# Kernel optimization log

Hardware: AMD Instinct MI355X
Metric: run time of the kernel (lower is better)

## Reference

```python
import jax, jax.numpy as jnp
import numpy as np

# static config (mirrors params)
T, B, NA, NF = 48, 256, 23, 4
D = NA * NF          # y_dim = 92
XD = 2               # x_dim
H = 128              # rnn_dim
HD = 128             # h_dim
NL = 2               # n_layers
FS = 0.1
BURN = 12
IN_ENC = XD + D + H  # GRU input size = 222
A0, A1 = 12, 11      # agents 0..11 -> net0, 12..22 -> net1


def setup_inputs() -> dict:
    key = jax.random.key(0)
    ks = jax.random.split(key, 16)
    s = 0.05
    rn = lambda k, shape: jax.random.normal(k, shape, jnp.float32) * s
    return {
        "states": jax.random.normal(ks[0], (T + 1, 1, B, D), jnp.float32),
        # per-network (leading dim 2) GRU layer-0 and layer-1 weights (torch GRU layout: [r|z|n])
        "W_ih0": rn(ks[1], (2, 3 * H, IN_ENC)),
        "W_hh0": rn(ks[2], (2, 3 * H, H)),
        "b_ih0": rn(ks[3], (2, 3 * H)),
        "b_hh0": rn(ks[4], (2, 3 * H)),
        "W_ih1": rn(ks[5], (2, 3 * H, H)),
        "W_hh1": rn(ks[6], (2, 3 * H, H)),
        "b_ih1": rn(ks[7], (2, 3 * H)),
        "b_hh1": rn(ks[8], (2, 3 * H)),
        # decoder MLP (dropout is identity in eval) + mean head
        "W1": rn(ks[9], (2, HD, H)),
        "b1": rn(ks[10], (2, HD)),
        "W2": rn(ks[11], (2, HD, HD)),
        "b2": rn(ks[12], (2, HD)),
        "Wm": rn(ks[13], (2, XD, HD)),
        "bm": rn(ks[14], (2, XD)),
        "rollout": 0,
        "train": 0,
    }


def _gru_cell(x, h, Wih, Whh, bih, bhh):
    gi = x @ Wih.T + bih
    gh = h @ Whh.T + bhh
    r = jax.nn.sigmoid(gi[:, :H] + gh[:, :H])
    z = jax.nn.sigmoid(gi[:, H:2 * H] + gh[:, H:2 * H])
    n = jnp.tanh(gi[:, 2 * H:] + r * gh[:, 2 * H:])
    return (1.0 - z) * n + z * h


def _batch_error(a, b):
    # sum over batch of the euclidean norm over features
    return jnp.sum(jnp.sqrt(jnp.sum((a - b) ** 2, axis=1)))


def _group_step(h, y_t, y3, y3n, lo, hi, g, P):
    # h: [NL, A*B, H]; agents lo..hi-1 of network g, folded into the batch dim
    A = hi - lo
    vel = y3[:, lo:hi, 2:4].transpose(1, 0, 2).reshape(A * B, 2)
    pos = y3[:, lo:hi, 0:2].transpose(1, 0, 2).reshape(A * B, 2)
    vel_true = y3n[:, lo:hi, 2:4].transpose(1, 0, 2).reshape(A * B, 2)
    pos_true = y3n[:, lo:hi, 0:2].transpose(1, 0, 2).reshape(A * B, 2)
    y_rep = jnp.broadcast_to(y_t[None], (A, B, D)).reshape(A * B, D)
    h_last = h[-1]
    enc_in = jnp.concatenate([vel, y_rep, h_last], axis=1)  # [A*B, IN_ENC]
    # decoder uses the PRE-update hidden state
    d = jax.nn.relu(h_last @ P["W1"][g].T + P["b1"][g])
    d = jax.nn.relu(d @ P["W2"][g].T + P["b2"][g])
    dm = d @ P["Wm"][g].T + P["bm"][g]  # [A*B, XD]
    # 2-layer GRU step
    h0n = _gru_cell(enc_in, h[0], P["W_ih0"][g], P["W_hh0"][g], P["b_ih0"][g], P["b_hh0"][g])
    h1n = _gru_cell(h0n, h[1], P["W_ih1"][g], P["W_hh1"][g], P["b_ih1"][g], P["b_hh1"][g])
    h_new = jnp.stack([h0n, h1n])
    L = _batch_error(dm, vel_true)
    ep = _batch_error(pos + vel * FS, pos_true)
    ev = _batch_error(dm[:, :2], vel_true)
    return h_new, L, ep, ev


def _forward(states, P):
    y_seq = states[:T, 0]       # [T, B, D]
    y_next = states[1:T + 1, 0]  # [T, B, D]

    def step(carry, xs):
        h0, h1, L, ep, ev = carry
        y_t, y_t1, t = xs
        y3 = y_t.reshape(B, NA, NF)
        y3n = y_t1.reshape(B, NA, NF)
        h0n, L0, ep0, ev0 = _group_step(h0, y_t, y3, y3n, 0, A0, 0, P)
        h1n, L1, ep1, ev1 = _group_step(h1, y_t, y3, y3n, A0, NA, 1, P)
        m = (t >= BURN).astype(jnp.float32)
        return (h0n, h1n, L + L0 + L1, ep + m * (ep0 + ep1), ev + m * (ev0 + ev1)), None

    init = (jnp.zeros((NL, A0 * B, H), jnp.float32),
            jnp.zeros((NL, A1 * B, H), jnp.float32),
            jnp.zeros((), jnp.float32), jnp.zeros((), jnp.float32), jnp.zeros((), jnp.float32))
    (h0, h1, L, ep, ev), _ = jax.lax.scan(step, init, (y_seq, y_next, jnp.arange(T)))
    L_rec = L / (T * NA)
    e_pos = ep / ((T - BURN) * NA)
    e_vel = ev / ((T - BURN) * NA)
    return L_rec, e_pos, e_vel


def reference(states, W_ih0, W_hh0, b_ih0, b_hh0, W_ih1, W_hh1, b_ih1, b_hh1,
              W1, b1, W2, b2, Wm, bm, rollout, train):
    P = dict(W_ih0=W_ih0, W_hh0=W_hh0, b_ih0=b_ih0, b_hh0=b_hh0,
             W_ih1=W_ih1, W_hh1=W_hh1, b_ih1=b_ih1, b_hh1=b_hh1,
             W1=W1, b1=b1, W2=W2, b2=b2, Wm=Wm, bm=bm)
    return _forward(states, P)
```

## Files before the change

### kernel.cpp

```cpp
#include <hip/hip_runtime.h>
#include <hip/hip_bf16.h>


typedef unsigned short u16;
typedef unsigned int u32;
typedef unsigned char u8;
typedef long i64;
typedef __attribute__((ext_vector_type(4))) float f32x4;

#define MFMA_F8(acc, a, b) (acc) = __builtin_amdgcn_mfma_f32_16x16x32_fp8_fp8((i64)(a), (i64)(b), (acc), 0, 0, 0)

__device__ __forceinline__ void pinA(i64& x) { asm volatile("" : "+a"(x)); }

__device__ __forceinline__ u8 f2e4(float v) {
  return (u8)(__builtin_amdgcn_cvt_pk_fp8_f32(v, 0.f, 0, false) & 0xff);
}
__device__ __forceinline__ u32 pk4(float a, float b, float c, float d) {
  u32 p = (u32)__builtin_amdgcn_cvt_pk_fp8_f32(a, b, 0, false);
  return (u32)__builtin_amdgcn_cvt_pk_fp8_f32(c, d, (int)p, true);
}
__device__ __forceinline__ float sigf(float x) {
  return __builtin_amdgcn_rcpf(1.f + __expf(-x));
}
__device__ __forceinline__ float tanh_fast(float x) {
  return 1.f - 2.f * __builtin_amdgcn_rcpf(1.f + __expf(2.f * x));
}

constexpr int E0 = 2 * 384 * 352;
constexpr int E1 = E0 + 2 * 384 * 256;
constexpr int E2 = E1 + 2 * 128 * 128;
constexpr int E3 = E2 + 2 * 128 * 128;
constexpr int E4 = E3 + 2 * 128 * 128;
constexpr int E5 = E4 + 2 * 128 * 128;
constexpr int NBIAS = 2048;
constexpr int TOTAL = E5 + NBIAS + 4;
constexpr int WB_BYTE_OFF = 16384;

constexpr int WYA_REL = E5;
constexpr int YBG_REL = WYA_REL + 23 * 384 * 96;
constexpr int NA1 = TOTAL;
constexpr int NA2 = NA1 + 23 * 384 * 96;
constexpr int NA3 = NA2 + 48 * 256 * 96;

__global__ void prep_kernel(const float* __restrict__ states,
                            const float* __restrict__ Wih0, const float* __restrict__ Whh0,
                            const float* __restrict__ bih0, const float* __restrict__ bhh0,
                            const float* __restrict__ Wih1, const float* __restrict__ Whh1,
                            const float* __restrict__ bih1, const float* __restrict__ bhh1,
                            const float* __restrict__ W1, const float* __restrict__ W2,
                            u8* __restrict__ wb, float* __restrict__ wsf) {
  for (int idx = blockIdx.x * blockDim.x + threadIdx.x; idx < NA3;
       idx += gridDim.x * blockDim.x) {
    if (idx < E0) {
      int g = idx / 135168;
      int r = idx - g * 135168;
      int j = r / 352;
      int k = r - j * 352;
      const float* wi = Wih0 + (g * 384 + j) * 222;
      float v;
      if (k < 94) v = wi[k];
      else if (k < 96) v = 0.f;
      else if (k < 224) v = wi[k - 2];
      else v = Whh0[(g * 384 + j) * 128 + (k - 224)];
      wb[idx] = f2e4(v);
    } else if (idx < E1) {
      int q = idx - E0;
      int g = q / 98304;
      int r = q - g * 98304;
      int j = r >> 8;
      int k = r & 255;
      float v = (k < 128) ? Wih1[(g * 384 + j) * 128 + k]
                          : Whh1[(g * 384 + j) * 128 + (k - 128)];
      wb[idx] = f2e4(v);
    } else if (idx < E2) {
      int q = idx - E1; int g = q >> 14; int r = q & 16383; int j = r >> 7; int k = r & 127;
      wb[idx] = f2e4(Whh0[(g * 384 + 256 + j) * 128 + k]);
    } else if (idx < E3) {
      int q = idx - E2; int g = q >> 14; int r = q & 16383; int j = r >> 7; int k = r & 127;
      wb[idx] = f2e4(Whh1[(g * 384 + 256 + j) * 128 + k]);
    } else if (idx < E4) {
      int q = idx - E3; int g = q >> 14; int r = q & 16383; int j = r >> 7; int k = r & 127;
      wb[idx] = f2e4(W1[(g * 128 + j) * 128 + k]);
    } else if (idx < E5) {
      int q = idx - E4; int g = q >> 14; int r = q & 16383; int j = r >> 7; int k = r & 127;
      wb[idx] = f2e4(W2[(g * 128 + j) * 128 + k]);
    } else if (idx < E5 + NBIAS) {
      int q = idx - E5;
      float v;
      if (q < 512)       { int g = q >> 8, j = q & 255;              v = bih0[g*384 + j] + bhh0[g*384 + j]; }
      else if (q < 768)  { int p = q - 512;  int g = p >> 7, j = p & 127; v = bih0[g*384 + 256 + j]; }
      else if (q < 1024) { int p = q - 768;  int g = p >> 7, j = p & 127; v = bhh0[g*384 + 256 + j]; }
      else if (q < 1536) { int p = q - 1024; int g = p >> 8, j = p & 255; v = bih1[g*384 + j] + bhh1[g*384 + j]; }
      else if (q < 1792) { int p = q - 1536; int g = p >> 7, j = p & 127; v = bih1[g*384 + 256 + j]; }
      else               { int p = q - 1792; int g = p >> 7, j = p & 127; v = bhh1[g*384 + 256 + j]; }
      wsf[4 + q] = v;
    } else if (idx < TOTAL) {
      wsf[idx - (E5 + NBIAS)] = 0.f;
    } else if (idx < NA2) {
      int q = idx - NA1;
      int a = q / 36864;
      int r = q - a * 36864;
      int j = r / 96;
      int k = r - j * 96;
      const float* wi = Wih0 + (((a >= 12) ? 1 : 0) * 384 + j) * 222;
      float v = (k < 92) ? wi[2 + k] : 0.f;
      if (k == a * 4 + 2) v += wi[0];
      if (k == a * 4 + 3) v += wi[1];
      wb[WYA_REL + q] = f2e4(v);
    } else {
      int q = idx - NA2;
      int t = q / 24576;
      int r = q - t * 24576;
      int row = r / 96;
      int k = r - row * 96;
      float v = (k < 92) ? states[((size_t)t * 256 + row) * 92 + k] : 0.f;
      wb[YBG_REL + q] = f2e4(v);
    }
  }
}

__global__ __launch_bounds__(512, 2) __attribute__((amdgpu_waves_per_eu(2, 2)))
void rnn_kernel(const float* __restrict__ states,
                const u8* __restrict__ wb,
                float* __restrict__ wsf,
                const float* __restrict__ b1g,
                const float* __restrict__ b2g,
                const float* __restrict__ Wmg,
                const float* __restrict__ bmg) {
  const int blk = blockIdx.x;
  const int g = (blk < 96) ? 0 : 1;
  const int r0 = (g == 0) ? (blk * 32) : ((blk - 96) * 32);
  const int aAg = (g == 0 ? 0 : 12) + (r0 >> 8);
  const int b0 = r0 & 255;

  const int tid = threadIdx.x;
  const int wid = tid >> 6;
  const int ln = tid & 63;
  const int j_in = ln & 15;
  const int kq = ln >> 4;
  const int c0 = wid * 16 + kq * 4;
  const int jh = wid * 16 + j_in;

  __shared__ __align__(16) u8 h0b[2][32 * 136];
  __shared__ __align__(16) u8 h1b[2][32 * 136];
  __shared__ __align__(16) u8 d1b[32 * 136];
  __shared__ __align__(16) u8 d2b[32 * 136];
  __shared__ __align__(16) float bias[1536];
  __shared__ float dmv[32][2];
  __shared__ float red[32][3];

  const u8* W0   = wb + g * 135168;
  const u8* W1c  = wb + E0 + g * 98304;
  const u8* Wn0p = wb + E1 + g * 16384;
  const u8* Wn1p = wb + E2 + g * 16384;
  const u8* Wm1p = wb + E3 + g * 16384;
  const u8* Wm2p = wb + E4 + g * 16384;
  const u8* WYA  = wb + WYA_REL + aAg * 36864;
  const u8* YBG  = wb + YBG_REL;

  i64 w0r[11], w0z[11], w0n[7];
#pragma unroll
  for (int kt = 0; kt < 3; ++kt) {
    w0r[kt] = *(const i64*)(WYA + (jh)       * 96 + kt * 32 + kq * 8);
    w0z[kt] = *(const i64*)(WYA + (128 + jh) * 96 + kt * 32 + kq * 8);
    w0n[kt] = *(const i64*)(WYA + (256 + jh) * 96 + kt * 32 + kq * 8);
  }
#pragma unroll
  for (int kt = 3; kt < 11; ++kt) {
    w0r[kt] = *(const i64*)(W0 + (jh)       * 352 + kt * 32 + kq * 8);
    w0z[kt] = *(const i64*)(W0 + (128 + jh) * 352 + kt * 32 + kq * 8);
    if (kt < 7) w0n[kt] = *(const i64*)(W0 + (256 + jh) * 352 + kt * 32 + kq * 8);
  }
  i64 w1r[8], w1z[8], w1n[4];
#pragma unroll
  for (int kt = 0; kt < 8; ++kt) {
    w1r[kt] = *(const i64*)(W1c + (jh)       * 256 + kt * 32 + kq * 8);
    w1z[kt] = *(const i64*)(W1c + (128 + jh) * 256 + kt * 32 + kq * 8);
    if (kt < 4) w1n[kt] = *(const i64*)(W1c + (256 + jh) * 256 + kt * 32 + kq * 8);
  }
  i64 wn0[4], wn1[4], wm1[4], wm2[4];
#pragma unroll
  for (int kt = 0; kt < 4; ++kt) {
    wn0[kt] = *(const i64*)(Wn0p + jh * 128 + kt * 32 + kq * 8);
    wn1[kt] = *(const i64*)(Wn1p + jh * 128 + kt * 32 + kq * 8);
    wm1[kt] = *(const i64*)(Wm1p + jh * 128 + kt * 32 + kq * 8);
    wm2[kt] = *(const i64*)(Wm2p + jh * 128 + kt * 32 + kq * 8);
  }
#pragma unroll
  for (int kt = 0; kt < 11; ++kt) { pinA(w0r[kt]); pinA(w0z[kt]); }
#pragma unroll
  for (int kt = 0; kt < 7; ++kt) pinA(w0n[kt]);
#pragma unroll
  for (int kt = 0; kt < 8; ++kt) { pinA(w1r[kt]); pinA(w1z[kt]); }
#pragma unroll
  for (int kt = 0; kt < 4; ++kt) {
    pinA(w1n[kt]); pinA(wn0[kt]); pinA(wn1[kt]); pinA(wm1[kt]); pinA(wm2[kt]);
  }

  for (int i = tid; i < 1536; i += 512) {
    float v;
    if (i < 256)       v = wsf[4 + g * 256 + i];
    else if (i < 384)  v = wsf[516 + g * 128 + (i - 256)];
    else if (i < 512)  v = wsf[772 + g * 128 + (i - 384)];
    else if (i < 768)  v = wsf[1028 + g * 256 + (i - 512)];
    else if (i < 896)  v = wsf[1540 + g * 128 + (i - 768)];
    else if (i < 1024) v = wsf[1796 + g * 128 + (i - 896)];
    else if (i < 1152) v = b1g[g * 128 + (i - 1024)];
    else if (i < 1280) v = b2g[g * 128 + (i - 1152)];
    else               v = Wmg[g * 256 + (i - 1280)];
    bias[i] = v;
  }
  for (int i = tid; i < 32 * 136; i += 512) { h0b[0][i] = 0; h1b[0][i] = 0; }

  const float bm0 = bmg[g * 2], bm1 = bmg[g * 2 + 1];
  f32x4 hv0[2] = {{0,0,0,0},{0,0,0,0}};
  f32x4 hv1[2] = {{0,0,0,0},{0,0,0,0}};
  float accL = 0.f, accEp = 0.f, accEv = 0.f;
  __syncthreads();

  for (int t = 0; t < 48; ++t) {
    const int cur = t & 1, nxt = cur ^ 1;
    const u8* h0c = h0b[cur]; u8* h0n = h0b[nxt];
    const u8* h1c = h1b[cur]; u8* h1n = h1b[nxt];

    const u8* yt = YBG + t * 24576;
    i64 yf[3][2];
#pragma unroll
    for (int kt = 0; kt < 3; ++kt) {
      yf[kt][0] = *(const i64*)(yt + (b0 + j_in) * 96 + kt * 32 + kq * 8);
      yf[kt][1] = *(const i64*)(yt + (b0 + 16 + j_in) * 96 + kt * 32 + kq * 8);
    }
    float sx=0, sy=0, svx=0, svy=0, nx=0, ny=0, nvx=0, nvy=0;
    if (tid < 32) {
      int te = (t > 0) ? (t - 1) : 0;
      const float* sr = states + ((size_t)(te * 256 + b0 + tid)) * 92 + aAg * 4;
      const float* sn = sr + 256 * 92;
      sx = sr[0]; sy = sr[1]; svx = sr[2]; svy = sr[3];
      nx = sn[0]; ny = sn[1]; nvx = sn[2]; nvy = sn[3];
    }

    const u8* pH1a = h1c + j_in * 136 + kq * 8;
    const u8* pH1b = h1c + (16 + j_in) * 136 + kq * 8;
    const u8* pH0a = h0c + j_in * 136 + kq * 8;
    const u8* pH0b = h0c + (16 + j_in) * 136 + kq * 8;

    i64 fh1[4][2];
#pragma unroll
    for (int kt = 0; kt < 4; ++kt) {
      fh1[kt][0] = *(const i64*)(pH1a + kt * 32);
      fh1[kt][1] = *(const i64*)(pH1b + kt * 32);
    }

    {
      f32x4 m0 = {0,0,0,0}, m1 = {0,0,0,0};
#pragma unroll
      for (int kt = 0; kt < 4; ++kt) {
        MFMA_F8(m0, wm1[kt], fh1[kt][0]);
        MFMA_F8(m1, wm1[kt], fh1[kt][1]);
      }
      f32x4 b1v = *(const f32x4*)(bias + 1024 + c0);
      *(u32*)(d1b + j_in * 136 + c0) =
        pk4(fmaxf(m0[0]+b1v[0],0.f), fmaxf(m0[1]+b1v[1],0.f), fmaxf(m0[2]+b1v[2],0.f), fmaxf(m0[3]+b1v[3],0.f));
      *(u32*)(d1b + (16 + j_in) * 136 + c0) =
        pk4(fmaxf(m1[0]+b1v[0],0.f), fmaxf(m1[1]+b1v[1],0.f), fmaxf(m1[2]+b1v[2],0.f), fmaxf(m1[3]+b1v[3],0.f));
    }

    {
      f32x4 aR[2] = {{0,0,0,0},{0,0,0,0}};
      f32x4 aZ[2] = {{0,0,0,0},{0,0,0,0}};
      f32x4 aN[2] = {{0,0,0,0},{0,0,0,0}};
      f32x4 aG[2] = {{0,0,0,0},{0,0,0,0}};
#pragma unroll
      for (int kt = 0; kt < 11; ++kt) {
        i64 bb0, bb1;
        if (kt < 3)      { bb0 = yf[kt][0];      bb1 = yf[kt][1]; }
        else if (kt < 7) { bb0 = fh1[kt - 3][0]; bb1 = fh1[kt - 3][1]; }
        else             { bb0 = *(const i64*)(pH0a + (kt - 7) * 32);
                           bb1 = *(const i64*)(pH0b + (kt - 7) * 32); }
        MFMA_F8(aR[0], w0r[kt], bb0); MFMA_F8(aR[1], w0r[kt], bb1);
        MFMA_F8(aZ[0], w0z[kt], bb0); MFMA_F8(aZ[1], w0z[kt], bb1);
        if (kt < 7) { MFMA_F8(aN[0], w0n[kt], bb0); MFMA_F8(aN[1], w0n[kt], bb1); }
        else        { MFMA_F8(aG[0], wn0[kt - 7], bb0); MFMA_F8(aG[1], wn0[kt - 7], bb1); }
      }
      f32x4 brv = *(const f32x4*)(bias + c0);
      f32x4 bzv = *(const f32x4*)(bias + 128 + c0);
      f32x4 biv = *(const f32x4*)(bias + 256 + c0);
      f32x4 bhv = *(const f32x4*)(bias + 384 + c0);
#pragma unroll
      for (int nt = 0; nt < 2; ++nt)
#pragma unroll
        for (int i = 0; i < 4; ++i) {
          float rv = sigf(aR[nt][i] + brv[i]);
          float zv = sigf(aZ[nt][i] + bzv[i]);
          float nv = tanh_fast(aN[nt][i] + biv[i] + rv * (aG[nt][i] + bhv[i]));
          hv0[nt][i] = (1.f - zv) * nv + zv * hv0[nt][i];
        }
#pragma unroll
      for (int nt = 0; nt < 2; ++nt)
        *(u32*)(h0n + (nt * 16 + j_in) * 136 + c0) = pk4(hv0[nt][0], hv0[nt][1], hv0[nt][2], hv0[nt][3]);
    }

    {
      int row = tid >> 4, c = (tid >> 3) & 1, part = tid & 7;
      const u8* dp = d2b + row * 136 + part * 16;
      const float* wmr = bias + 1280 + c * 128 + part * 16;
      float s = 0.f;
#pragma unroll
      for (int q = 0; q < 4; ++q) {
        u32 w = *(const u32*)(dp + q * 4);
        s += wmr[q * 4 + 0] * __builtin_amdgcn_cvt_f32_fp8((int)w, 0);
        s += wmr[q * 4 + 1] * __builtin_amdgcn_cvt_f32_fp8((int)w, 1);
        s += wmr[q * 4 + 2] * __builtin_amdgcn_cvt_f32_fp8((int)w, 2);
        s += wmr[q * 4 + 3] * __builtin_amdgcn_cvt_f32_fp8((int)w, 3);
      }
      s += __shfl_xor(s, 1); s += __shfl_xor(s, 2); s += __shfl_xor(s, 4);
      if (part == 0) dmv[row][c] = s;
    }
    __syncthreads();

    if (t > 0 && tid < 32) {
      float dx = dmv[tid][0] + bm0 - nvx;
      float dy = dmv[tid][1] + bm1 - nvy;
      float e = sqrtf(dx * dx + dy * dy);
      accL += e;
      if (t - 1 >= 12) {
        accEv += e;
        float ex = sx + 0.1f * svx - nx;
        float ey = sy + 0.1f * svy - ny;
        accEp += sqrtf(ex * ex + ey * ey);
      }
    }

    {
      f32x4 m0 = {0,0,0,0}, m1 = {0,0,0,0};
#pragma unroll
      for (int kt = 0; kt < 4; ++kt) {
        i64 bb0 = *(const i64*)(d1b + j_in * 136 + kt * 32 + kq * 8);
        i64 bb1 = *(const i64*)(d1b + (16 + j_in) * 136 + kt * 32 + kq * 8);
        MFMA_F8(m0, wm2[kt], bb0);
        MFMA_F8(m1, wm2[kt], bb1);
      }
      f32x4 b2v = *(const f32x4*)(bias + 1152 + c0);
      *(u32*)(d2b + j_in * 136 + c0) =
        pk4(fmaxf(m0[0]+b2v[0],0.f), fmaxf(m0[1]+b2v[1],0.f), fmaxf(m0[2]+b2v[2],0.f), fmaxf(m0[3]+b2v[3],0.f));
      *(u32*)(d2b + (16 + j_in) * 136 + c0) =
        pk4(fmaxf(m1[0]+b2v[0],0.f), fmaxf(m1[1]+b2v[1],0.f), fmaxf(m1[2]+b2v[2],0.f), fmaxf(m1[3]+b2v[3],0.f));
    }

    {
      f32x4 aR[2] = {{0,0,0,0},{0,0,0,0}};
      f32x4 aZ[2] = {{0,0,0,0},{0,0,0,0}};
      f32x4 aN[2] = {{0,0,0,0},{0,0,0,0}};
      f32x4 aG[2] = {{0,0,0,0},{0,0,0,0}};
      const u8* pG0a = h0n + j_in * 136 + kq * 8;
      const u8* pG0b = h0n + (16 + j_in) * 136 + kq * 8;
#pragma unroll
      for (int kt = 0; kt < 8; ++kt) {
        i64 bb0, bb1;
        if (kt < 4) { bb0 = *(const i64*)(pG0a + kt * 32); bb1 = *(const i64*)(pG0b + kt * 32); }
        else        { bb0 = fh1[kt - 4][0];                bb1 = fh1[kt - 4][1]; }
        MFMA_F8(aR[0], w1r[kt], bb0); MFMA_F8(aR[1], w1r[kt], bb1);
        MFMA_F8(aZ[0], w1z[kt], bb0); MFMA_F8(aZ[1], w1z[kt], bb1);
        if (kt < 4) { MFMA_F8(aN[0], w1n[kt], bb0); MFMA_F8(aN[1], w1n[kt], bb1); }
        else        { MFMA_F8(aG[0], wn1[kt - 4], bb0); MFMA_F8(aG[1], wn1[kt - 4], bb1); }
      }
      f32x4 brv = *(const f32x4*)(bias + 512 + c0);
      f32x4 bzv = *(const f32x4*)(bias + 640 + c0);
      f32x4 biv = *(const f32x4*)(bias + 768 + c0);
      f32x4 bhv = *(const f32x4*)(bias + 896 + c0);
#pragma unroll
      for (int nt = 0; nt < 2; ++nt)
#pragma unroll
        for (int i = 0; i < 4; ++i) {
          float rv = sigf(aR[nt][i] + brv[i]);
          float zv = sigf(aZ[nt][i] + bzv[i]);
          float nv = tanh_fast(aN[nt][i] + biv[i] + rv * (aG[nt][i] + bhv[i]));
          hv1[nt][i] = (1.f - zv) * nv + zv * hv1[nt][i];
        }
#pragma unroll
      for (int nt = 0; nt < 2; ++nt)
        *(u32*)(h1n + (nt * 16 + j_in) * 136 + c0) = pk4(hv1[nt][0], hv1[nt][1], hv1[nt][2], hv1[nt][3]);
    }
    __syncthreads();
  }

  {
    int row = tid >> 4, c = (tid >> 3) & 1, part = tid & 7;
    const u8* dp = d2b + row * 136 + part * 16;
    const float* wmr = bias + 1280 + c * 128 + part * 16;
    float s = 0.f;
#pragma unroll
    for (int q = 0; q < 4; ++q) {
      u32 w = *(const u32*)(dp + q * 4);
      s += wmr[q * 4 + 0] * __builtin_amdgcn_cvt_f32_fp8((int)w, 0);
      s += wmr[q * 4 + 1] * __builtin_amdgcn_cvt_f32_fp8((int)w, 1);
      s += wmr[q * 4 + 2] * __builtin_amdgcn_cvt_f32_fp8((int)w, 2);
      s += wmr[q * 4 + 3] * __builtin_amdgcn_cvt_f32_fp8((int)w, 3);
    }
    s += __shfl_xor(s, 1); s += __shfl_xor(s, 2); s += __shfl_xor(s, 4);
    if (part == 0) dmv[row][c] = s;
  }
  __syncthreads();
  if (tid < 32) {
    const float* sr = states + ((size_t)(47 * 256 + b0 + tid)) * 92 + aAg * 4;
    const float* sn = sr + 256 * 92;
    float dx = dmv[tid][0] + bm0 - sn[2];
    float dy = dmv[tid][1] + bm1 - sn[3];
    float e = sqrtf(dx * dx + dy * dy);
    accL += e;
    accEv += e;
    float ex = sr[0] + 0.1f * sr[2] - sn[0];
    float ey = sr[1] + 0.1f * sr[3] - sn[1];
    accEp += sqrtf(ex * ex + ey * ey);
    red[tid][0] = accL; red[tid][1] = accEp; red[tid][2] = accEv;
  }
  __syncthreads();
  if (tid < 3) {
    float s = 0.f;
    for (int i = 0; i < 32; ++i) s += red[i][tid];
    atomicAdd(&wsf[tid], s);
  }
}

__global__ void fin_kernel(const float* __restrict__ wacc, float* __restrict__ out) {
  if (threadIdx.x == 0 && blockIdx.x == 0) {
    out[0] = wacc[0] / 1104.f;
    out[1] = wacc[1] / 828.f;
    out[2] = wacc[2] / 828.f;
  }
}

extern "C" void kernel_launch(void* const* d_in, const int* in_sizes, int n_in,
                              void* d_out, int out_size, void* d_ws, size_t ws_size,
                              hipStream_t stream) {
  const float* states = (const float*)d_in[0];
  const float* Wih0 = (const float*)d_in[1];
  const float* Whh0 = (const float*)d_in[2];
  const float* bih0 = (const float*)d_in[3];
  const float* bhh0 = (const float*)d_in[4];
  const float* Wih1 = (const float*)d_in[5];
  const float* Whh1 = (const float*)d_in[6];
  const float* bih1 = (const float*)d_in[7];
  const float* bhh1 = (const float*)d_in[8];
  const float* W1   = (const float*)d_in[9];
  const float* b1   = (const float*)d_in[10];
  const float* W2   = (const float*)d_in[11];
  const float* b2   = (const float*)d_in[12];
  const float* Wm   = (const float*)d_in[13];
  const float* bm   = (const float*)d_in[14];

  float* wsf = (float*)d_ws;
  u8* wb = (u8*)d_ws + WB_BYTE_OFF;

  int prep_blocks = (NA3 + 255) / 256;
  if (prep_blocks > 2048) prep_blocks = 2048;
  prep_kernel<<<prep_blocks, 256, 0, stream>>>(states, Wih0, Whh0, bih0, bhh0,
                                               Wih1, Whh1, bih1, bhh1,
                                               W1, W2, wb, wsf);
  rnn_kernel<<<184, 512, 0, stream>>>(states, wb, wsf, b1, b2, Wm, bm);
  fin_kernel<<<1, 64, 0, stream>>>(wsf, (float*)d_out);
}
```

Before: 338.3 us.

## Defer loss computation to epilogue and reload decoder weights per step

The per-step decoder mean-head outputs are stored in a shared [48][32][2] buffer, and all error and loss accumulation moves to one epilogue that is parallelised over the whole block and reduced with wave shuffles. This takes the per-step global state loads and the serial tid<32 tail out of the recurrent loop. The decoder MLP weights are no longer pinned in accumulator registers and are reloaded from global memory every step. The mean-head dot product is moved between the layer-1 MFMAs and their gate math, and a barrier is added after the second decoder layer. These changes lower register pressure and shorten the critical path, in exchange for more global loads and one extra barrier per step.

```diff
diff --git a/kernel.cpp b/kernel.cpp
--- a/kernel.cpp
+++ b/kernel.cpp
@@ -146,8 +146,8 @@
   __shared__ __align__(16) u8 d1b[32 * 136];
   __shared__ __align__(16) u8 d2b[32 * 136];
   __shared__ __align__(16) float bias[1536];
-  __shared__ float dmv[32][2];
-  __shared__ float red[32][3];
+  __shared__ float dmv[48][32][2];
+  __shared__ float red[8][3];
 
   const u8* W0   = wb + g * 135168;
   const u8* W1c  = wb + E0 + g * 98304;
@@ -178,13 +178,11 @@
     w1z[kt] = *(const i64*)(W1c + (128 + jh) * 256 + kt * 32 + kq * 8);
     if (kt < 4) w1n[kt] = *(const i64*)(W1c + (256 + jh) * 256 + kt * 32 + kq * 8);
   }
-  i64 wn0[4], wn1[4], wm1[4], wm2[4];
+  i64 wn0[4], wn1[4];
 #pragma unroll
   for (int kt = 0; kt < 4; ++kt) {
     wn0[kt] = *(const i64*)(Wn0p + jh * 128 + kt * 32 + kq * 8);
     wn1[kt] = *(const i64*)(Wn1p + jh * 128 + kt * 32 + kq * 8);
-    wm1[kt] = *(const i64*)(Wm1p + jh * 128 + kt * 32 + kq * 8);
-    wm2[kt] = *(const i64*)(Wm2p + jh * 128 + kt * 32 + kq * 8);
   }
 #pragma unroll
   for (int kt = 0; kt < 11; ++kt) { pinA(w0r[kt]); pinA(w0z[kt]); }
@@ -193,9 +191,7 @@
 #pragma unroll
   for (int kt = 0; kt < 8; ++kt) { pinA(w1r[kt]); pinA(w1z[kt]); }
 #pragma unroll
-  for (int kt = 0; kt < 4; ++kt) {
-    pinA(w1n[kt]); pinA(wn0[kt]); pinA(wn1[kt]); pinA(wm1[kt]); pinA(wm2[kt]);
-  }
+  for (int kt = 0; kt < 4; ++kt) { pinA(w1n[kt]); pinA(wn0[kt]); pinA(wn1[kt]); }
 
   for (int i = tid; i < 1536; i += 512) {
     float v;
@@ -212,10 +208,8 @@
   }
   for (int i = tid; i < 32 * 136; i += 512) { h0b[0][i] = 0; h1b[0][i] = 0; }
 
-  const float bm0 = bmg[g * 2], bm1 = bmg[g * 2 + 1];
   f32x4 hv0[2] = {{0,0,0,0},{0,0,0,0}};
   f32x4 hv1[2] = {{0,0,0,0},{0,0,0,0}};
-  float accL = 0.f, accEp = 0.f, accEv = 0.f;
   __syncthreads();
 
   for (int t = 0; t < 48; ++t) {
@@ -230,14 +224,6 @@
       yf[kt][0] = *(const i64*)(yt + (b0 + j_in) * 96 + kt * 32 + kq * 8);
       yf[kt][1] = *(const i64*)(yt + (b0 + 16 + j_in) * 96 + kt * 32 + kq * 8);
     }
-    float sx=0, sy=0, svx=0, svy=0, nx=0, ny=0, nvx=0, nvy=0;
-    if (tid < 32) {
-      int te = (t > 0) ? (t - 1) : 0;
-      const float* sr = states + ((size_t)(te * 256 + b0 + tid)) * 92 + aAg * 4;
-      const float* sn = sr + 256 * 92;
-      sx = sr[0]; sy = sr[1]; svx = sr[2]; svy = sr[3];
-      nx = sn[0]; ny = sn[1]; nvx = sn[2]; nvy = sn[3];
-    }
 
     const u8* pH1a = h1c + j_in * 136 + kq * 8;
     const u8* pH1b = h1c + (16 + j_in) * 136 + kq * 8;
@@ -255,8 +241,9 @@
       f32x4 m0 = {0,0,0,0}, m1 = {0,0,0,0};
 #pragma unroll
       for (int kt = 0; kt < 4; ++kt) {
-        MFMA_F8(m0, wm1[kt], fh1[kt][0]);
-        MFMA_F8(m1, wm1[kt], fh1[kt][1]);
+        i64 w = *(const i64*)(Wm1p + jh * 128 + kt * 32 + kq * 8);
+        MFMA_F8(m0, w, fh1[kt][0]);
+        MFMA_F8(m1, w, fh1[kt][1]);
       }
       f32x4 b1v = *(const f32x4*)(bias + 1024 + c0);
       *(u32*)(d1b + j_in * 136 + c0) =
@@ -295,50 +282,21 @@
           float nv = tanh_fast(aN[nt][i] + biv[i] + rv * (aG[nt][i] + bhv[i]));
           hv0[nt][i] = (1.f - zv) * nv + zv * hv0[nt][i];
         }
-#pragma unroll
-      for (int nt = 0; nt < 2; ++nt)
-        *(u32*)(h0n + (nt * 16 + j_in) * 136 + c0) = pk4(hv0[nt][0], hv0[nt][1], hv0[nt][2], hv0[nt][3]);
-    }
-
-    {
-      int row = tid >> 4, c = (tid >> 3) & 1, part = tid & 7;
-      const u8* dp = d2b + row * 136 + part * 16;
-      const float* wmr = bias + 1280 + c * 128 + part * 16;
-      float s = 0.f;
-#pragma unroll
-      for (int q = 0; q < 4; ++q) {
-        u32 w = *(const u32*)(dp + q * 4);
-        s += wmr[q * 4 + 0] * __builtin_amdgcn_cvt_f32_fp8((int)w, 0);
-        s += wmr[q * 4 + 1] * __builtin_amdgcn_cvt_f32_fp8((int)w, 1);
-        s += wmr[q * 4 + 2] * __builtin_amdgcn_cvt_f32_fp8((int)w, 2);
-        s += wmr[q * 4 + 3] * __builtin_amdgcn_cvt_f32_fp8((int)w, 3);
-      }
-      s += __shfl_xor(s, 1); s += __shfl_xor(s, 2); s += __shfl_xor(s, 4);
-      if (part == 0) dmv[row][c] = s;
     }
     __syncthreads();
 
-    if (t > 0 && tid < 32) {
-      float dx = dmv[tid][0] + bm0 - nvx;
-      float dy = dmv[tid][1] + bm1 - nvy;
-      float e = sqrtf(dx * dx + dy * dy);
-      accL += e;
-      if (t - 1 >= 12) {
-        accEv += e;
-        float ex = sx + 0.1f * svx - nx;
-        float ey = sy + 0.1f * svy - ny;
-        accEp += sqrtf(ex * ex + ey * ey);
-      }
-    }
-
+#pragma unroll
+    for (int nt = 0; nt < 2; ++nt)
+      *(u32*)(h0n + (nt * 16 + j_in) * 136 + c0) = pk4(hv0[nt][0], hv0[nt][1], hv0[nt][2], hv0[nt][3]);
     {
       f32x4 m0 = {0,0,0,0}, m1 = {0,0,0,0};
 #pragma unroll
       for (int kt = 0; kt < 4; ++kt) {
+        i64 w = *(const i64*)(Wm2p + jh * 128 + kt * 32 + kq * 8);
         i64 bb0 = *(const i64*)(d1b + j_in * 136 + kt * 32 + kq * 8);
         i64 bb1 = *(const i64*)(d1b + (16 + j_in) * 136 + kt * 32 + kq * 8);
-        MFMA_F8(m0, wm2[kt], bb0);
-        MFMA_F8(m1, wm2[kt], bb1);
+        MFMA_F8(m0, w, bb0);
+        MFMA_F8(m1, w, bb1);
       }
       f32x4 b2v = *(const f32x4*)(bias + 1152 + c0);
       *(u32*)(d2b + j_in * 136 + c0) =
@@ -346,6 +304,7 @@
       *(u32*)(d2b + (16 + j_in) * 136 + c0) =
         pk4(fmaxf(m1[0]+b2v[0],0.f), fmaxf(m1[1]+b2v[1],0.f), fmaxf(m1[2]+b2v[2],0.f), fmaxf(m1[3]+b2v[3],0.f));
     }
+    __syncthreads();
 
     {
       f32x4 aR[2] = {{0,0,0,0},{0,0,0,0}};
@@ -364,6 +323,22 @@
         if (kt < 4) { MFMA_F8(aN[0], w1n[kt], bb0); MFMA_F8(aN[1], w1n[kt], bb1); }
         else        { MFMA_F8(aG[0], wn1[kt - 4], bb0); MFMA_F8(aG[1], wn1[kt - 4], bb1); }
       }
+      {
+        int row = tid >> 4, c = (tid >> 3) & 1, part = tid & 7;
+        const u8* dp = d2b + row * 136 + part * 16;
+        const float* wmr = bias + 1280 + c * 128 + part * 16;
+        float s = 0.f;
+#pragma unroll
+        for (int q = 0; q < 4; ++q) {
+          u32 w = *(const u32*)(dp + q * 4);
+          s += wmr[q * 4 + 0] * __builtin_amdgcn_cvt_f32_fp8((int)w, 0);
+          s += wmr[q * 4 + 1] * __builtin_amdgcn_cvt_f32_fp8((int)w, 1);
+          s += wmr[q * 4 + 2] * __builtin_amdgcn_cvt_f32_fp8((int)w, 2);
+          s += wmr[q * 4 + 3] * __builtin_amdgcn_cvt_f32_fp8((int)w, 3);
+        }
+        s += __shfl_xor(s, 1); s += __shfl_xor(s, 2); s += __shfl_xor(s, 4);
+        if (part == 0) dmv[t][row][c] = s;
+      }
       f32x4 brv = *(const f32x4*)(bias + 512 + c0);
       f32x4 bzv = *(const f32x4*)(bias + 640 + c0);
       f32x4 biv = *(const f32x4*)(bias + 768 + c0);
@@ -384,40 +359,34 @@
     __syncthreads();
   }
 
-  {
-    int row = tid >> 4, c = (tid >> 3) & 1, part = tid & 7;
-    const u8* dp = d2b + row * 136 + part * 16;
-    const float* wmr = bias + 1280 + c * 128 + part * 16;
-    float s = 0.f;
-#pragma unroll
-    for (int q = 0; q < 4; ++q) {
-      u32 w = *(const u32*)(dp + q * 4);
-      s += wmr[q * 4 + 0] * __builtin_amdgcn_cvt_f32_fp8((int)w, 0);
-      s += wmr[q * 4 + 1] * __builtin_amdgcn_cvt_f32_fp8((int)w, 1);
-      s += wmr[q * 4 + 2] * __builtin_amdgcn_cvt_f32_fp8((int)w, 2);
-      s += wmr[q * 4 + 3] * __builtin_amdgcn_cvt_f32_fp8((int)w, 3);
-    }
-    s += __shfl_xor(s, 1); s += __shfl_xor(s, 2); s += __shfl_xor(s, 4);
-    if (part == 0) dmv[row][c] = s;
-  }
-  __syncthreads();
-  if (tid < 32) {
-    const float* sr = states + ((size_t)(47 * 256 + b0 + tid)) * 92 + aAg * 4;
+  float accL = 0.f, accEp = 0.f, accEv = 0.f;
+  const float bm0 = bmg[g * 2], bm1 = bmg[g * 2 + 1];
+  for (int idx = tid; idx < 1536; idx += 512) {
+    int t = idx >> 5, row = idx & 31;
+    const float* sr = states + ((size_t)(t * 256 + b0 + row)) * 92 + aAg * 4;
     const float* sn = sr + 256 * 92;
-    float dx = dmv[tid][0] + bm0 - sn[2];
-    float dy = dmv[tid][1] + bm1 - sn[3];
+    float dx = dmv[t][row][0] + bm0 - sn[2];
+    float dy = dmv[t][row][1] + bm1 - sn[3];
     float e = sqrtf(dx * dx + dy * dy);
     accL += e;
-    accEv += e;
-    float ex = sr[0] + 0.1f * sr[2] - sn[0];
-    float ey = sr[1] + 0.1f * sr[3] - sn[1];
-    accEp += sqrtf(ex * ex + ey * ey);
-    red[tid][0] = accL; red[tid][1] = accEp; red[tid][2] = accEv;
-  }
+    if (t >= 12) {
+      accEv += e;
+      float ex = sr[0] + 0.1f * sr[2] - sn[0];
+      float ey = sr[1] + 0.1f * sr[3] - sn[1];
+      accEp += sqrtf(ex * ex + ey * ey);
+    }
+  }
+#pragma unroll
+  for (int k = 1; k < 64; k <<= 1) {
+    accL  += __shfl_xor(accL, k);
+    accEp += __shfl_xor(accEp, k);
+    accEv += __shfl_xor(accEv, k);
+  }
+  if (ln == 0) { red[wid][0] = accL; red[wid][1] = accEp; red[wid][2] = accEv; }
   __syncthreads();
   if (tid < 3) {
     float s = 0.f;
-    for (int i = 0; i < 32; ++i) s += red[i][tid];
+    for (int i = 0; i < 8; ++i) s += red[i][tid];
     atomicAdd(&wsf[tid], s);
   }
 }
```

After: 357.3 us. +5.6%, slower.
